# Optimization experiments

Measured on AMD Instinct MI355X. Metric: run time of the kernel, lower is better.

## Reference

```python
import jax, jax.numpy as jnp
import numpy as np

B, S, T = 32, 400, 64
V, E, H = 32000, 256, 512


def _lstm_step(x, h, c, W_ih, W_hh, b):
    # PyTorch LSTM gate order: i, f, g, o
    g = x @ W_ih.T + h @ W_hh.T + b
    i, f, gg, o = jnp.split(g, 4, axis=-1)
    i = jax.nn.sigmoid(i)
    f = jax.nn.sigmoid(f)
    gg = jnp.tanh(gg)
    o = jax.nn.sigmoid(o)
    c_new = f * c + i * gg
    h_new = o * jnp.tanh(c_new)
    return h_new, c_new


def setup_inputs() -> dict:
    key = jax.random.key(0)
    ks = jax.random.split(key, 32)
    d = {}
    d['src'] = jax.random.randint(ks[0], (B, S), 1, V)
    d['src_lengths'] = jnp.full((B,), S, dtype=jnp.int32)
    d['tgt'] = jax.random.randint(ks[1], (B, T), 1, V)
    sc = 0.05
    emb = jax.random.normal(ks[2], (V, E), jnp.float32) * sc
    d['emb'] = emb.at[0].set(0.0)  # padding_idx=0
    d['enc_W_ih_f'] = jax.random.normal(ks[3], (4 * H, E), jnp.float32) * sc
    d['enc_W_hh_f'] = jax.random.normal(ks[4], (4 * H, H), jnp.float32) * sc
    d['enc_b_ih_f'] = jax.random.normal(ks[5], (4 * H,), jnp.float32) * sc
    d['enc_b_hh_f'] = jax.random.normal(ks[6], (4 * H,), jnp.float32) * sc
    d['enc_W_ih_b'] = jax.random.normal(ks[7], (4 * H, E), jnp.float32) * sc
    d['enc_W_hh_b'] = jax.random.normal(ks[8], (4 * H, H), jnp.float32) * sc
    d['enc_b_ih_b'] = jax.random.normal(ks[9], (4 * H,), jnp.float32) * sc
    d['enc_b_hh_b'] = jax.random.normal(ks[10], (4 * H,), jnp.float32) * sc
    d['enc_init_h'] = jax.random.uniform(ks[11], (2, H), jnp.float32, -0.01, 0.01)
    d['enc_init_c'] = jax.random.uniform(ks[12], (2, H), jnp.float32, -0.01, 0.01)
    d['dec_h_W'] = jax.random.normal(ks[13], (H, 2 * H), jnp.float32) * sc
    d['dec_c_W'] = jax.random.normal(ks[14], (H, 2 * H), jnp.float32) * sc
    d['cell_W_ih'] = jax.random.normal(ks[15], (4 * H, E), jnp.float32) * sc
    d['cell_W_hh'] = jax.random.normal(ks[16], (4 * H, H), jnp.float32) * sc
    d['cell_b_ih'] = jax.random.normal(ks[17], (4 * H,), jnp.float32) * sc
    d['cell_b_hh'] = jax.random.normal(ks[18], (4 * H,), jnp.float32) * sc
    d['attn_W'] = jax.random.normal(ks[19], (H, 2 * H), jnp.float32) * sc
    d['attn_b'] = jax.random.normal(ks[20], (H,), jnp.float32) * sc
    d['concat_W'] = jax.random.normal(ks[21], (H, 3 * H), jnp.float32) * sc
    d['concat_b'] = jax.random.normal(ks[22], (H,), jnp.float32) * sc
    d['out_W'] = jax.random.normal(ks[23], (V, H), jnp.float32) * sc
    d['out_b'] = jax.random.normal(ks[24], (V,), jnp.float32) * sc
    return d


def reference(src, src_lengths, tgt, emb,
              enc_W_ih_f, enc_W_hh_f, enc_b_ih_f, enc_b_hh_f,
              enc_W_ih_b, enc_W_hh_b, enc_b_ih_b, enc_b_hh_b,
              enc_init_h, enc_init_c, dec_h_W, dec_c_W,
              cell_W_ih, cell_W_hh, cell_b_ih, cell_b_hh,
              attn_W, attn_b, concat_W, concat_b, out_W, out_b):
    Bs, Ss = src.shape
    Hs = enc_init_h.shape[1]
    xe = emb[src].transpose(1, 0, 2)  # [S, B, E]

    # ---- bi-LSTM encoder (all lengths == S, so packing is identity) ----
    h0f = jnp.broadcast_to(enc_init_h[0], (Bs, Hs))
    c0f = jnp.broadcast_to(enc_init_c[0], (Bs, Hs))
    h0b = jnp.broadcast_to(enc_init_h[1], (Bs, Hs))
    c0b = jnp.broadcast_to(enc_init_c[1], (Bs, Hs))

    def enc_fwd(carry, x):
        h, c = carry
        h, c = _lstm_step(x, h, c, enc_W_ih_f, enc_W_hh_f, enc_b_ih_f + enc_b_hh_f)
        return (h, c), h

    def enc_bwd(carry, x):
        h, c = carry
        h, c = _lstm_step(x, h, c, enc_W_ih_b, enc_W_hh_b, enc_b_ih_b + enc_b_hh_b)
        return (h, c), h

    (hf, cf), out_f = jax.lax.scan(enc_fwd, (h0f, c0f), xe)
    (hb, cb), out_b_seq = jax.lax.scan(enc_bwd, (h0b, c0b), xe[::-1])
    out_b_seq = out_b_seq[::-1]
    enc_outs = jnp.concatenate([out_f, out_b_seq], axis=-1)  # [S, B, 2H]

    # bridge final states to decoder init
    dec_h = jnp.concatenate([hf, hb], axis=-1) @ dec_h_W.T  # [B, H]
    dec_c = jnp.concatenate([cf, cb], axis=-1) @ dec_c_W.T

    mask = jnp.arange(Ss)[None, :] < src_lengths[:, None]  # [B, S]
    attn_keys = enc_outs @ attn_W.T + attn_b  # [S, B, H]

    def dec_step(carry, t_ids):
        h, c = carry
        x = emb[t_ids]  # [B, E]
        h, c = _lstm_step(x, h, c, cell_W_ih, cell_W_hh, cell_b_ih + cell_b_hh)
        scores = jnp.einsum('bh,sbh->bs', h, attn_keys)
        scores = jnp.where(mask, scores, jnp.float32(-1e18))
        w = jax.nn.softmax(scores, axis=1)  # [B, S]
        context = jnp.einsum('bs,sbd->bd', w, enc_outs)  # [B, 2H]
        cc = jnp.tanh(jnp.concatenate([context, h], axis=-1) @ concat_W.T + concat_b)
        logit = jax.nn.log_softmax(cc @ out_W.T + out_b, axis=-1)  # [B, V]
        return (h, c), logit

    _, logits = jax.lax.scan(dec_step, (dec_h, dec_c), tgt.T)  # [T, B, V]
    return logits.transpose(1, 0, 2)  # [B, T, V]
```

## Files before the change

kernel.cpp:

```cpp
#include <hip/hip_runtime.h>
#include <math.h>

#define BB 32
#define SS 400
#define TT 64
#define VV 32000
#define EE 256
#define HH 512

typedef __attribute__((ext_vector_type(4))) float f32x4;
typedef __attribute__((ext_vector_type(8))) short bf16x8t;
typedef __attribute__((ext_vector_type(8))) unsigned short u16x8;
typedef __attribute__((ext_vector_type(4))) unsigned int u32x4;
typedef unsigned long long u64t;

__device__ __forceinline__ ushort f2bf(float x) {
  uint u = __float_as_uint(x);
  return (ushort)((u + 0x7fffu + ((u >> 16) & 1u)) >> 16);
}
__device__ __forceinline__ float bf2f(ushort x) {
  return __uint_as_float(((uint)x) << 16);
}
__device__ __forceinline__ void gload_lds16(const ushort* g, ushort* l) {
  __builtin_amdgcn_global_load_lds(
      (const __attribute__((address_space(1))) void*)g,
      (__attribute__((address_space(3))) void*)l, 16, 0, 0);
}
__device__ __forceinline__ void unpack8(uint4 u, float* f) {
  f[0] = __uint_as_float(u.x << 16); f[1] = __uint_as_float(u.x & 0xffff0000u);
  f[2] = __uint_as_float(u.y << 16); f[3] = __uint_as_float(u.y & 0xffff0000u);
  f[4] = __uint_as_float(u.z << 16); f[5] = __uint_as_float(u.z & 0xffff0000u);
  f[6] = __uint_as_float(u.w << 16); f[7] = __uint_as_float(u.w & 0xffff0000u);
}

__global__ __launch_bounds__(256) void init_all_kernel(
    const float* __restrict__ einh, uint* __restrict__ hge,
    uint* __restrict__ hgb)
{
  int i = blockIdx.x * 256 + threadIdx.x;
  if (i < 4096) {
    int c = (i & 127) * 4;
    uint lo = (uint)f2bf(einh[c]) | ((uint)f2bf(einh[c + 1]) << 16);
    uint hi = (uint)f2bf(einh[c + 2]) | ((uint)f2bf(einh[c + 3]) << 16);
    u32x4 pkt = {lo, hi, 0u, 0u};
    *(u32x4*)(hge + (size_t)i * 4) = pkt;
  } else if (i < 8192) {
    int p = i - 4096;
    int c = HH + (p & 127) * 4;
    uint lo = (uint)f2bf(einh[c]) | ((uint)f2bf(einh[c + 1]) << 16);
    uint hi = (uint)f2bf(einh[c + 2]) | ((uint)f2bf(einh[c + 3]) << 16);
    u32x4 pkt = {lo, hi, 0u, 0u};
    *(u32x4*)(hgb + (size_t)p * 4) = pkt;
  }
}

__global__ __launch_bounds__(256) void f2bf_kernel(
    const float* __restrict__ in, ushort* __restrict__ out, long n)
{
  long step = (long)gridDim.x * 256 * 4;
  for (long i = ((long)blockIdx.x * 256 + threadIdx.x) * 4; i < n; i += step) {
    float4 v = *(const float4*)(in + i);
    ushort4 o;
    o.x = f2bf(v.x); o.y = f2bf(v.y); o.z = f2bf(v.z); o.w = f2bf(v.w);
    *(ushort4*)(out + i) = o;
  }
}

__global__ __launch_bounds__(64) void gather_x_kernel(
    const float* __restrict__ emb, const int* __restrict__ tok, int L,
    ushort* __restrict__ xout)
{
  int row = blockIdx.x;
  int b = row & 31, s = row >> 5;
  int t = tok[b * L + s];
  float4 v = ((const float4*)(emb + (size_t)t * EE))[threadIdx.x];
  ushort4 o;
  o.x = f2bf(v.x); o.y = f2bf(v.y); o.z = f2bf(v.z); o.w = f2bf(v.w);
  ((ushort4*)(xout + (size_t)row * EE))[threadIdx.x] = o;
}

__global__ __launch_bounds__(256) void bias3_kernel(
    const float* a1, const float* a2, const float* b1, const float* b2,
    const float* c1, const float* c2, float* out)
{
  int i = blockIdx.x * 256 + threadIdx.x;
  if (i < 2048) out[i] = a1[i] + a2[i];
  else if (i < 4096) out[i] = b1[i - 2048] + b2[i - 2048];
  else if (i < 6144) out[i] = c1[i - 4096] + c2[i - 4096];
}

__global__ __launch_bounds__(256) void gemm_mfma_kernel(
    const ushort* __restrict__ A, const ushort* __restrict__ B,
    const float* __restrict__ bias, void* __restrict__ Cout,
    int M, int N, int K, int flags)
{
  __shared__ ushort Asub[128 * 32], Bsub[128 * 32];
  int tid = threadIdx.x;
  int w = tid >> 6, l = tid & 63;
  int n0 = blockIdx.x * 128, m0 = blockIdx.y * 128;
  int wm = w >> 1, wn = w & 1;

  int srow = 16 * 2 * w + (l >> 2);
  int scol = (l & 3) * 8;
  const ushort* Ar0 = A + (size_t)(m0 + srow) * K + scol;
  const ushort* Ar1 = Ar0 + (size_t)16 * K;
  const ushort* Br0 = B + (size_t)(n0 + srow) * K + scol;
  const ushort* Br1 = Br0 + (size_t)16 * K;
  ushort* ldsA0 = Asub + (2 * w) * 512;
  ushort* ldsA1 = Asub + (2 * w + 1) * 512;
  ushort* ldsB0 = Bsub + (2 * w) * 512;
  ushort* ldsB1 = Bsub + (2 * w + 1) * 512;

  f32x4 acc[4][4];
  #pragma unroll
  for (int i = 0; i < 4; ++i)
    #pragma unroll
    for (int j = 0; j < 4; ++j)
      acc[i][j] = (f32x4){0.f, 0.f, 0.f, 0.f};

  int lr = l & 15, lkb = (l >> 4) * 8;

  for (int k0 = 0; k0 < K; k0 += 32) {
    gload_lds16(Ar0 + k0, ldsA0);
    gload_lds16(Ar1 + k0, ldsA1);
    gload_lds16(Br0 + k0, ldsB0);
    gload_lds16(Br1 + k0, ldsB1);
    __syncthreads();
    bf16x8t af[4], bfv[4];
    #pragma unroll
    for (int mf = 0; mf < 4; ++mf)
      af[mf] = *(const bf16x8t*)&Asub[(wm * 64 + mf * 16 + lr) * 32 + lkb];
    #pragma unroll
    for (int nf = 0; nf < 4; ++nf)
      bfv[nf] = *(const bf16x8t*)&Bsub[(wn * 64 + nf * 16 + lr) * 32 + lkb];
    #pragma unroll
    for (int mf = 0; mf < 4; ++mf)
      #pragma unroll
      for (int nf = 0; nf < 4; ++nf)
        acc[mf][nf] = __builtin_amdgcn_mfma_f32_16x16x32_bf16(
            af[mf], bfv[nf], acc[mf][nf], 0, 0, 0);
    __syncthreads();
  }

  int lg = l >> 4;
  #pragma unroll
  for (int mf = 0; mf < 4; ++mf) {
    #pragma unroll
    for (int nf = 0; nf < 4; ++nf) {
      int n = n0 + wn * 64 + nf * 16 + lr;
      float bv = bias[n];
      #pragma unroll
      for (int r = 0; r < 4; ++r) {
        int m = m0 + wm * 64 + mf * 16 + lg * 4 + r;
        float v = acc[mf][nf][r] + bv;
        if (flags & 1) v = tanhf(v);
        if (flags & 8) {
          int s = m >> 5, b = m & 31;
          int gate = n >> 9, col = n & 511;
          size_t dst = (((size_t)s * 32 + (col >> 4)) * 32 + b) * 64 +
                       (size_t)(col & 15) * 4 + gate;
          ((ushort*)Cout)[dst] = f2bf(v);
        } else {
          int row = (flags & 2) ? ((m & 31) * TT + (m >> 5)) : m;
          if (flags & 4) ((ushort*)Cout)[(size_t)row * N + n] = f2bf(v);
          else           ((float*)Cout)[(size_t)row * N + n] = v;
        }
      }
    }
  }
}

struct PersistArgs {
  const float* W_hh;
  const ushort* xw;
  uint* hpack;
  const float* c_init_elem;
  const float* c_init_bcast;
  ushort* out_h;
  int out_os, out_ofs;
  int steps, backward;
  float* h_final;
  float* c_final;
};

__global__ __launch_bounds__(256) void lstm_persist_kernel(
    PersistArgs A0, PersistArgs A1, int nblk_dir)
{
  __shared__ ushort ldsW[64 * 512];
  __shared__ ushort ldsH[32 * 512];
  __shared__ ushort ldsX[32 * 64];

  PersistArgs a = ((int)blockIdx.x < nblk_dir) ? A0 : A1;
  int cblk = (int)blockIdx.x % nblk_dir;
  int c0 = cblk * 16;
  int tid = threadIdx.x;
  int w = tid >> 6, l = tid & 63;
  int lr = l & 15, kb = (l >> 4) * 8;
  int g = l & 3;
  int col = c0 + w * 4 + (lr >> 2);
  int n = w * 16 + lr;

  {
    int nn = tid >> 2;
    int kbase = (tid & 3) * 128;
    int rW = (nn & 3) * HH + c0 + (nn >> 2);
    const float4* src = (const float4*)(a.W_hh + (size_t)rW * HH + kbase);
    #pragma unroll
    for (int j = 0; j < 16; ++j) {
      float4 u = src[2 * j], v = src[2 * j + 1];
      u16x8 o;
      o[0] = f2bf(u.x); o[1] = f2bf(u.y); o[2] = f2bf(u.z); o[3] = f2bf(u.w);
      o[4] = f2bf(v.x); o[5] = f2bf(v.y); o[6] = f2bf(v.z); o[7] = f2bf(v.w);
      int k = kbase + j * 8;
      int byte = (nn * 1024 + k * 2) ^ ((nn & 7) << 4);
      *(u16x8*)((char*)ldsW + byte) = o;
    }
  }

  float creg[2][4];
  #pragma unroll
  for (int mf = 0; mf < 2; ++mf)
    #pragma unroll
    for (int r = 0; r < 4; ++r) {
      int b = mf * 16 + (l >> 4) * 4 + r;
      creg[mf][r] = a.c_init_bcast ? a.c_init_bcast[col]
                                   : a.c_init_elem[b * HH + col];
    }
  __syncthreads();

  int prow0 = tid >> 7;
  int pcp4 = tid & 127;

  int s0i = a.backward ? (a.steps - 1) : 0;
  float4 xcur = *(const float4*)(a.xw + ((size_t)s0i * 32 + cblk) * 2048 + tid * 8);
  float4 xnext;

  for (int it = 0; it < a.steps; ++it) {
    int s = a.backward ? (a.steps - 1 - it) : it;
    const uint* hsrc = a.hpack + (size_t)(it & 1) * 4096 * 4;
    uint* hdst = a.hpack + (size_t)((it + 1) & 1) * 4096 * 4;

    u32x4 pv[16];
    {
      int guard = 0;
      while (true) {
        #pragma unroll
        for (int j = 0; j < 16; ++j) {
          const uint* ap = hsrc + (size_t)((prow0 + 2 * j) * 128 + pcp4) * 4;
          asm volatile("global_load_dwordx4 %0, %1, off sc0 sc1"
                       : "=v"(pv[j]) : "v"(ap) : "memory");
        }
        asm volatile("s_waitcnt vmcnt(0)" ::: "memory");
        __builtin_amdgcn_sched_barrier(0);
        uint bad = 0;
        #pragma unroll
        for (int j = 0; j < 16; ++j) bad |= (pv[j][2] ^ (uint)it);
        if (bad == 0) break;
        if (++guard > (1 << 18)) break;
        __builtin_amdgcn_s_sleep(1);
      }
    }
    __syncthreads();

    #pragma unroll
    for (int j = 0; j < 16; ++j) {
      int row = prow0 + 2 * j;
      int byte = (row * 1024 + pcp4 * 8) ^ ((row & 7) << 4);
      *(u64t*)((char*)ldsH + byte) = ((u64t)pv[j][1] << 32) | (u64t)pv[j][0];
    }
    *(float4*)&ldsX[tid * 8] = xcur;
    __syncthreads();

    f32x4 acc0 = (f32x4){0.f, 0.f, 0.f, 0.f};
    f32x4 acc1 = (f32x4){0.f, 0.f, 0.f, 0.f};
    #pragma unroll
    for (int k0 = 0; k0 < HH; k0 += 32) {
      int ka = k0 + kb;
      bf16x8t av0 = *(const bf16x8t*)((const char*)ldsH + ((lr * 1024 + ka * 2) ^ ((lr & 7) << 4)));
      bf16x8t av1 = *(const bf16x8t*)((const char*)ldsH + (((16 + lr) * 1024 + ka * 2) ^ (((16 + lr) & 7) << 4)));
      int wr = w * 16 + lr;
      bf16x8t bv = *(const bf16x8t*)((const char*)ldsW + ((wr * 1024 + ka * 2) ^ ((wr & 7) << 4)));
      acc0 = __builtin_amdgcn_mfma_f32_16x16x32_bf16(av0, bv, acc0, 0, 0, 0);
      acc1 = __builtin_amdgcn_mfma_f32_16x16x32_bf16(av1, bv, acc1, 0, 0, 0);
    }

    u64t pk[2][4];
    #pragma unroll
    for (int mf = 0; mf < 2; ++mf) {
      f32x4 ac = mf ? acc1 : acc0;
      #pragma unroll
      for (int r = 0; r < 4; ++r) {
        int b = mf * 16 + (l >> 4) * 4 + r;
        float v = ac[r] + bf2f(ldsX[b * 64 + n]);
        float b1 = __shfl_xor(v, 1);
        float b2 = __shfl_xor(v, 2);
        float b3 = __shfl_xor(v, 3);
        float hnew = 0.f;
        if (g == 0) {
          float iv = 1.f / (1.f + expf(-v));
          float fv = 1.f / (1.f + expf(-b1));
          float gv = tanhf(b2);
          float ov = 1.f / (1.f + expf(-b3));
          float cnew = fv * creg[mf][r] + iv * gv;
          hnew = ov * tanhf(cnew);
          creg[mf][r] = cnew;
          if (a.h_final && it == a.steps - 1) {
            a.h_final[b * HH + col] = hnew;
            a.c_final[b * HH + col] = cnew;
          }
        }
        uint hu = (uint)f2bf(hnew);
        uint p1 = __shfl_xor(hu, 4);
        uint p2 = __shfl_xor(hu, 8);
        uint p3 = __shfl_xor(p1, 8);
        uint lo = hu | (p1 << 16);
        uint hi = p2 | (p3 << 16);
        pk[mf][r] = ((u64t)hi << 32) | (u64t)lo;
      }
    }

    if ((l & 15) == 0 && it + 1 < a.steps) {
      int cp4w = cblk * 4 + w;
      #pragma unroll
      for (int mf = 0; mf < 2; ++mf)
        #pragma unroll
        for (int r = 0; r < 4; ++r) {
          int b = mf * 16 + (l >> 4) * 4 + r;
          u32x4 pkt;
          pkt[0] = (uint)pk[mf][r];
          pkt[1] = (uint)(pk[mf][r] >> 32);
          pkt[2] = (uint)(it + 1);
          pkt[3] = 0u;
          uint* dp = hdst + (size_t)(b * 128 + cp4w) * 4;
          asm volatile("global_store_dwordx4 %0, %1, off sc0 sc1"
                       :: "v"(dp), "v"(pkt) : "memory");
        }
    }

    if ((l & 15) == 0) {
      #pragma unroll
      for (int mf = 0; mf < 2; ++mf)
        #pragma unroll
        for (int r = 0; r < 4; ++r) {
          int b = mf * 16 + (l >> 4) * 4 + r;
          *(u64t*)(a.out_h + (size_t)s * BB * a.out_os + b * a.out_os +
                   a.out_ofs + c0 + w * 4) = pk[mf][r];
        }
    }
    if (it + 1 < a.steps) {
      int sn = a.backward ? (a.steps - 2 - it) : (it + 1);
      const ushort* xp = a.xw + ((size_t)sn * 32 + cblk) * 2048 + tid * 8;
      asm volatile("global_load_dwordx4 %0, %1, off"
                   : "=v"(xnext) : "v"(xp) : "memory");
    }
    xcur = xnext;
  }
}

__global__ __launch_bounds__(256) void dec_init_kernel(
    const float* __restrict__ hf, const float* __restrict__ hb,
    const float* __restrict__ cf, const float* __restrict__ cb,
    const float* __restrict__ Wh, const float* __restrict__ Wc,
    uint* __restrict__ dh_pack, float* __restrict__ dc)
{
  int b = blockIdx.x;
  __shared__ float hcat[2 * HH], ccat[2 * HH];
  __shared__ ushort dhs[HH];
  int tid = threadIdx.x;
  for (int i = tid; i < HH; i += 256) {
    hcat[i] = hf[b * HH + i]; hcat[HH + i] = hb[b * HH + i];
    ccat[i] = cf[b * HH + i]; ccat[HH + i] = cb[b * HH + i];
  }
  __syncthreads();
  for (int col = tid; col < HH; col += 256) {
    const float4* wh = (const float4*)(Wh + (size_t)col * (2 * HH));
    const float4* wc = (const float4*)(Wc + (size_t)col * (2 * HH));
    float ah = 0.f, acv = 0.f;
    #pragma unroll 4
    for (int k4 = 0; k4 < (2 * HH) / 4; ++k4) {
      float4 h4 = *(const float4*)&hcat[k4 * 4];
      float4 w4 = wh[k4];
      ah += h4.x * w4.x + h4.y * w4.y + h4.z * w4.z + h4.w * w4.w;
      float4 c4 = *(const float4*)&ccat[k4 * 4];
      float4 v4 = wc[k4];
      acv += c4.x * v4.x + c4.y * v4.y + c4.z * v4.z + c4.w * v4.w;
    }
    dhs[col] = f2bf(ah);
    dc[b * HH + col] = acv;
  }
  __syncthreads();
  if (tid < 128) {
    int c = tid * 4;
    uint lo = (uint)dhs[c] | ((uint)dhs[c + 1] << 16);
    uint hi = (uint)dhs[c + 2] | ((uint)dhs[c + 3] << 16);
    u32x4 pkt = {lo, hi, 0u, 0u};
    *(u32x4*)(dh_pack + (size_t)(b * 128 + tid) * 4) = pkt;
  }
}

__global__ __launch_bounds__(256) void scores_kernel(
    const ushort* __restrict__ keys_bf, const ushort* __restrict__ dhall,
    const int* __restrict__ slen, float* __restrict__ sc)
{
  int b = blockIdx.x & 31, s0 = ((int)blockIdx.x >> 5) * 16;
  __shared__ ushort ldsD[64][520];
  __shared__ ushort ldsK[16][520];
  int tid = threadIdx.x;
  #pragma unroll
  for (int j = 0; j < 16; ++j) {
    int ci = tid + 256 * j;
    int row = ci >> 6, c8 = (ci & 63) * 8;
    *(u16x8*)&ldsD[row][c8] = *(const u16x8*)(dhall + ((size_t)row * BB + b) * HH + c8);
  }
  #pragma unroll
  for (int j = 0; j < 4; ++j) {
    int ci = tid + 256 * j;
    int row = ci >> 6, c8 = (ci & 63) * 8;
    *(u16x8*)&ldsK[row][c8] = *(const u16x8*)(keys_bf + ((size_t)(s0 + row) * BB + b) * HH + c8);
  }
  __syncthreads();

  int sl = tid & 15, tq = tid >> 4;
  float acc[4] = {0.f, 0.f, 0.f, 0.f};
  for (int k8 = 0; k8 < 64; ++k8) {
    float kv[8];
    unpack8(*(const uint4*)&ldsK[sl][k8 * 8], kv);
    #pragma unroll
    for (int j = 0; j < 4; ++j) {
      float dv[8];
      unpack8(*(const uint4*)&ldsD[tq * 4 + j][k8 * 8], dv);
      #pragma unroll
      for (int e = 0; e < 8; ++e) acc[j] += kv[e] * dv[e];
    }
  }
  int s = s0 + sl;
  int len = slen[b];
  #pragma unroll
  for (int j = 0; j < 4; ++j) {
    int t = tq * 4 + j;
    sc[((size_t)t * BB + b) * SS + s] = (s < len) ? acc[j] : -1e18f;
  }
}

__global__ __launch_bounds__(64) void softmax_kernel(
    const float* __restrict__ sc, ushort* __restrict__ wbf)
{
  int row = blockIdx.x;
  int tid = threadIdx.x;
  float v[7];
  float m = -3e38f;
  #pragma unroll
  for (int j = 0; j < 7; ++j) {
    int s = tid + 64 * j;
    v[j] = (s < SS) ? sc[(size_t)row * SS + s] : -3e38f;
    m = fmaxf(m, v[j]);
  }
  #pragma unroll
  for (int o = 32; o; o >>= 1) m = fmaxf(m, __shfl_xor(m, o));
  float ssum = 0.f;
  float p[7];
  #pragma unroll
  for (int j = 0; j < 7; ++j) {
    int s = tid + 64 * j;
    p[j] = (s < SS) ? expf(v[j] - m) : 0.f;
    ssum += p[j];
  }
  #pragma unroll
  for (int o = 32; o; o >>= 1) ssum += __shfl_xor(ssum, o);
  float inv = 1.f / ssum;
  #pragma unroll
  for (int j = 0; j < 7; ++j) {
    int s = tid + 64 * j;
    if (s < 416) wbf[(size_t)row * 416 + s] = (s < SS) ? f2bf(p[j] * inv) : (ushort)0;
  }
}

__global__ __launch_bounds__(256) void context_kernel(
    const ushort* __restrict__ wbf, const ushort* __restrict__ enc,
    const ushort* __restrict__ dhall, ushort* __restrict__ catb)
{
  int b = blockIdx.x, ch = blockIdx.y;
  int tid = threadIdx.x;
  if (ch >= 16) {
    int c0 = (ch - 16) * 64;
    #pragma unroll
    for (int j = 0; j < 2; ++j) {
      int ci = tid + 256 * j;
      int t = ci >> 3, u = ci & 7;
      *(u16x8*)(catb + ((size_t)t * BB + b) * 1536 + 1024 + c0 + u * 8) =
          *(const u16x8*)(dhall + ((size_t)t * BB + b) * HH + c0 + u * 8);
    }
    return;
  }
  int d0 = ch * 64;
  __shared__ ushort ldsWt[64][424];
  for (int ci = tid; ci < 64 * 52; ci += 256) {
    int t = ci / 52, u = ci % 52;
    *(u16x8*)&ldsWt[t][u * 8] = *(const u16x8*)(wbf + (size_t)(t * BB + b) * 416 + u * 8);
  }
  __syncthreads();

  int d = d0 + (tid & 63), tq = tid >> 6;
  float acc16[16];
  #pragma unroll
  for (int i = 0; i < 16; ++i) acc16[i] = 0.f;

  for (int s8 = 0; s8 < 50; ++s8) {
    float ev[8];
    #pragma unroll
    for (int e = 0; e < 8; ++e)
      ev[e] = bf2f(enc[((size_t)(s8 * 8 + e) * BB + b) * 1024 + d]);
    #pragma unroll
    for (int i = 0; i < 16; ++i) {
      float wv[8];
      unpack8(*(const uint4*)&ldsWt[tq * 16 + i][s8 * 8], wv);
      #pragma unroll
      for (int e = 0; e < 8; ++e) acc16[i] += wv[e] * ev[e];
    }
  }
  #pragma unroll
  for (int i = 0; i < 16; ++i) {
    int t = tq * 16 + i;
    catb[((size_t)t * BB + b) * 1536 + d] = f2bf(acc16[i]);
  }
}

__global__ __launch_bounds__(1024) void logsoftmax_kernel(float* __restrict__ out)
{
  int r = blockIdx.x;
  __shared__ float row[VV];
  __shared__ float red[16];
  int tid = threadIdx.x;
  float4* p = (float4*)(out + (size_t)r * VV);
  float4* rp = (float4*)row;
  float m = -3e38f;
  #pragma unroll
  for (int j = 0; j < 8; ++j) {
    int i = tid + 1024 * j;
    if (i < VV / 4) {
      float4 v = p[i];
      rp[i] = v;
      m = fmaxf(m, fmaxf(fmaxf(v.x, v.y), fmaxf(v.z, v.w)));
    }
  }
  #pragma unroll
  for (int o = 32; o; o >>= 1) m = fmaxf(m, __shfl_xor(m, o));
  if ((tid & 63) == 0) red[tid >> 6] = m;
  __syncthreads();
  float mm = red[0];
  #pragma unroll
  for (int i = 1; i < 16; ++i) mm = fmaxf(mm, red[i]);
  __syncthreads();
  float ssum = 0.f;
  #pragma unroll
  for (int j = 0; j < 8; ++j) {
    int i = tid + 1024 * j;
    if (i < VV / 4) {
      float4 v = rp[i];
      ssum += expf(v.x - mm) + expf(v.y - mm) + expf(v.z - mm) + expf(v.w - mm);
    }
  }
  #pragma unroll
  for (int o = 32; o; o >>= 1) ssum += __shfl_xor(ssum, o);
  if ((tid & 63) == 0) red[tid >> 6] = ssum;
  __syncthreads();
  float st = red[0];
  #pragma unroll
  for (int i = 1; i < 16; ++i) st += red[i];
  st = mm + logf(st);
  #pragma unroll
  for (int j = 0; j < 8; ++j) {
    int i = tid + 1024 * j;
    if (i < VV / 4) {
      float4 v = rp[i];
      v.x -= st; v.y -= st; v.z -= st; v.w -= st;
      p[i] = v;
    }
  }
}

extern "C" void kernel_launch(void* const* d_in, const int* in_sizes, int n_in,
                              void* d_out, int out_size, void* d_ws, size_t ws_size,
                              hipStream_t stream)
{
  (void)in_sizes; (void)n_in; (void)out_size; (void)ws_size;
  const int*   src  = (const int*)d_in[0];
  const int*   slen = (const int*)d_in[1];
  const int*   tgt  = (const int*)d_in[2];
  const float* emb  = (const float*)d_in[3];
  const float* eWif = (const float*)d_in[4];
  const float* eWhf = (const float*)d_in[5];
  const float* ebif = (const float*)d_in[6];
  const float* ebhf = (const float*)d_in[7];
  const float* eWib = (const float*)d_in[8];
  const float* eWhb = (const float*)d_in[9];
  const float* ebib = (const float*)d_in[10];
  const float* ebhb = (const float*)d_in[11];
  const float* einh = (const float*)d_in[12];
  const float* einc = (const float*)d_in[13];
  const float* dhW  = (const float*)d_in[14];
  const float* dcW  = (const float*)d_in[15];
  const float* cWi  = (const float*)d_in[16];
  const float* cWh  = (const float*)d_in[17];
  const float* cbi  = (const float*)d_in[18];
  const float* cbh  = (const float*)d_in[19];
  const float* aW   = (const float*)d_in[20];
  const float* abv  = (const float*)d_in[21];
  const float* ccW  = (const float*)d_in[22];
  const float* ccbv = (const float*)d_in[23];
  const float* oW   = (const float*)d_in[24];
  const float* obv  = (const float*)d_in[25];
  float* out = (float*)d_out;
  float* ws  = (float*)d_ws;

  size_t off = 0;
  ushort* enc_bf  = (ushort*)(ws + off); off += (size_t)SS * BB * 1024 / 2;
  ushort* keys_bf = (ushort*)(ws + off); off += (size_t)SS * BB * HH / 2;
  ushort* dhall_bf= (ushort*)(ws + off); off += (size_t)TT * BB * HH / 2;
  ushort* catb_bf = (ushort*)(ws + off); off += (size_t)TT * BB * 1536 / 2;
  ushort* ccv_bf  = (ushort*)(ws + off); off += (size_t)TT * BB * HH / 2;
  float*  scbuf   = ws + off;            off += (size_t)TT * BB * SS;
  ushort* w_bf    = (ushort*)(ws + off); off += (size_t)TT * BB * 416 / 2;
  ushort* xe_bf   = (ushort*)(ws + off); off += (size_t)SS * BB * EE / 2;
  ushort* xd_bf   = (ushort*)(ws + off); off += (size_t)TT * BB * EE / 2;
  ushort* xWf_bf  = (ushort*)(ws + off); off += (size_t)SS * BB * 2048 / 2;
  ushort* xWb_bf  = (ushort*)(ws + off); off += (size_t)SS * BB * 2048 / 2;
  ushort* xWd_bf  = (ushort*)(ws + off); off += (size_t)TT * BB * 2048 / 2;
  ushort* oW_bf   = (ushort*)(ws + off); off += (size_t)VV * HH / 2;
  ushort* aW_bf   = (ushort*)(ws + off); off += (size_t)HH * 1024 / 2;
  ushort* ccW_bf  = (ushort*)(ws + off); off += (size_t)HH * 1536 / 2;
  ushort* eWif_bf = (ushort*)(ws + off); off += (size_t)2048 * EE / 2;
  ushort* eWib_bf = (ushort*)(ws + off); off += (size_t)2048 * EE / 2;
  ushort* cWi_bf  = (ushort*)(ws + off); off += (size_t)2048 * EE / 2;
  uint* hge_pack = (uint*)(ws + off); off += (size_t)2 * 4096 * 4;
  uint* hgb_pack = (uint*)(ws + off); off += (size_t)2 * 4096 * 4;
  uint* hdec_pack= (uint*)(ws + off); off += (size_t)2 * 4096 * 4;
  float* bias3 = ws + off; off += 3 * 2048;
  float* hf_f  = ws + off; off += BB * HH;
  float* hb_f  = ws + off; off += BB * HH;
  float* cf_f  = ws + off; off += BB * HH;
  float* cb_f  = ws + off; off += BB * HH;
  float* dcb   = ws + off; off += BB * HH;

  hipMemsetAsync(hge_pack, 0, (size_t)3 * 2 * 4096 * 16, stream);

  init_all_kernel<<<64, 256, 0, stream>>>(einh, hge_pack, hgb_pack);

  f2bf_kernel<<<2048, 256, 0, stream>>>(oW, oW_bf, (long)VV * HH);
  f2bf_kernel<<<512, 256, 0, stream>>>(aW, aW_bf, (long)HH * 1024);
  f2bf_kernel<<<512, 256, 0, stream>>>(ccW, ccW_bf, (long)HH * 1536);
  f2bf_kernel<<<512, 256, 0, stream>>>(eWif, eWif_bf, (long)2048 * EE);
  f2bf_kernel<<<512, 256, 0, stream>>>(eWib, eWib_bf, (long)2048 * EE);
  f2bf_kernel<<<512, 256, 0, stream>>>(cWi, cWi_bf, (long)2048 * EE);
  bias3_kernel<<<24, 256, 0, stream>>>(ebif, ebhf, ebib, ebhb, cbi, cbh, bias3);

  gather_x_kernel<<<SS * BB, 64, 0, stream>>>(emb, src, SS, xe_bf);
  gather_x_kernel<<<TT * BB, 64, 0, stream>>>(emb, tgt, TT, xd_bf);
  gemm_mfma_kernel<<<dim3(2048 / 128, (SS * BB) / 128), 256, 0, stream>>>(
      xe_bf, eWif_bf, bias3, xWf_bf, SS * BB, 2048, EE, 8);
  gemm_mfma_kernel<<<dim3(2048 / 128, (SS * BB) / 128), 256, 0, stream>>>(
      xe_bf, eWib_bf, bias3 + 2048, xWb_bf, SS * BB, 2048, EE, 8);
  gemm_mfma_kernel<<<dim3(2048 / 128, (TT * BB) / 128), 256, 0, stream>>>(
      xd_bf, cWi_bf, bias3 + 4096, xWd_bf, TT * BB, 2048, EE, 8);

  {
    PersistArgs af, ab;
    af.W_hh = eWhf; af.xw = xWf_bf; af.hpack = hge_pack;
    af.c_init_elem = nullptr; af.c_init_bcast = einc;
    af.out_h = enc_bf; af.out_os = 1024; af.out_ofs = 0;
    af.steps = SS; af.backward = 0;
    af.h_final = hf_f; af.c_final = cf_f;
    ab = af;
    ab.W_hh = eWhb; ab.xw = xWb_bf; ab.hpack = hgb_pack;
    ab.c_init_bcast = einc + HH;
    ab.out_ofs = HH; ab.backward = 1;
    ab.h_final = hb_f; ab.c_final = cb_f;
    lstm_persist_kernel<<<64, 256, 0, stream>>>(af, ab, 32);
  }

  dec_init_kernel<<<BB, 256, 0, stream>>>(hf_f, hb_f, cf_f, cb_f, dhW, dcW,
                                          hdec_pack, dcb);
  {
    PersistArgs ad;
    ad.W_hh = cWh; ad.xw = xWd_bf; ad.hpack = hdec_pack;
    ad.c_init_elem = dcb; ad.c_init_bcast = nullptr;
    ad.out_h = dhall_bf; ad.out_os = HH; ad.out_ofs = 0;
    ad.steps = TT; ad.backward = 0;
    ad.h_final = nullptr; ad.c_final = nullptr;
    lstm_persist_kernel<<<32, 256, 0, stream>>>(ad, ad, 32);
  }

  gemm_mfma_kernel<<<dim3(HH / 128, (SS * BB) / 128), 256, 0, stream>>>(
      enc_bf, aW_bf, abv, keys_bf, SS * BB, HH, 1024, 4);

  scores_kernel<<<32 * 25, 256, 0, stream>>>(keys_bf, dhall_bf, slen, scbuf);
  softmax_kernel<<<TT * BB, 64, 0, stream>>>(scbuf, w_bf);
  context_kernel<<<dim3(BB, 24), 256, 0, stream>>>(w_bf, enc_bf, dhall_bf, catb_bf);

  gemm_mfma_kernel<<<dim3(HH / 128, (TT * BB) / 128), 256, 0, stream>>>(
      catb_bf, ccW_bf, ccbv, ccv_bf, TT * BB, HH, 1536, 1 | 4);
  gemm_mfma_kernel<<<dim3(VV / 128, (TT * BB) / 128), 256, 0, stream>>>(
      ccv_bf, oW_bf, obv, out, TT * BB, VV, HH, 2);

  logsoftmax_kernel<<<TT * BB, 1024, 0, stream>>>(out);
}
```

Baseline: 3.548 ms.

## Use fast exp math, spread gate activations across lanes, poll per-row in encoder

Replaces expf/tanhf with __expf-based sigmoid and tanh in the LSTM cell and the softmax/log-softmax kernels. Each lane now applies its own gate activation before the shuffles, so the transcendental work is spread across four lanes instead of done serially on one. The spin-wait on the h exchange now issues all loads once and re-polls only the rows whose flag is stale, instead of reloading all sixteen. Fast exp lowers accuracy slightly, and the poll change alters synchronisation latency on the serial recurrence.

```diff
diff --git a/kernel.cpp b/kernel.cpp
--- a/kernel.cpp
+++ b/kernel.cpp
@@ -20,6 +20,12 @@
 }
 __device__ __forceinline__ float bf2f(ushort x) {
   return __uint_as_float(((uint)x) << 16);
+}
+__device__ __forceinline__ float fsigmoid(float x) {
+  return 1.f / (1.f + __expf(-x));
+}
+__device__ __forceinline__ float ftanh(float x) {
+  return 1.f - 2.f / (__expf(2.f * x) + 1.f);
 }
 __device__ __forceinline__ void gload_lds16(const ushort* g, ushort* l) {
   __builtin_amdgcn_global_load_lds(
@@ -241,23 +247,25 @@
     uint* hdst = a.hpack + (size_t)((it + 1) & 1) * 4096 * 4;
 
     u32x4 pv[16];
-    {
+    #pragma unroll
+    for (int j = 0; j < 16; ++j) {
+      const uint* ap = hsrc + (size_t)((prow0 + 2 * j) * 128 + pcp4) * 4;
+      asm volatile("global_load_dwordx4 %0, %1, off sc0 sc1"
+                   : "=v"(pv[j]) : "v"(ap) : "memory");
+    }
+    asm volatile("s_waitcnt vmcnt(0)" ::: "memory");
+    __builtin_amdgcn_sched_barrier(0);
+    #pragma unroll
+    for (int j = 0; j < 16; ++j) {
+      const uint* ap = hsrc + (size_t)((prow0 + 2 * j) * 128 + pcp4) * 4;
       int guard = 0;
-      while (true) {
-        #pragma unroll
-        for (int j = 0; j < 16; ++j) {
-          const uint* ap = hsrc + (size_t)((prow0 + 2 * j) * 128 + pcp4) * 4;
-          asm volatile("global_load_dwordx4 %0, %1, off sc0 sc1"
-                       : "=v"(pv[j]) : "v"(ap) : "memory");
-        }
-        asm volatile("s_waitcnt vmcnt(0)" ::: "memory");
+      while (pv[j][2] != (uint)it) {
+        __builtin_amdgcn_s_sleep(1);
+        asm volatile("global_load_dwordx4 %0, %1, off sc0 sc1\n\t"
+                     "s_waitcnt vmcnt(0)"
+                     : "=v"(pv[j]) : "v"(ap) : "memory");
         __builtin_amdgcn_sched_barrier(0);
-        uint bad = 0;
-        #pragma unroll
-        for (int j = 0; j < 16; ++j) bad |= (pv[j][2] ^ (uint)it);
-        if (bad == 0) break;
-        if (++guard > (1 << 18)) break;
-        __builtin_amdgcn_s_sleep(1);
+        if (++guard > (1 << 20)) break;
       }
     }
     __syncthreads();
@@ -292,17 +300,15 @@
       for (int r = 0; r < 4; ++r) {
         int b = mf * 16 + (l >> 4) * 4 + r;
         float v = ac[r] + bf2f(ldsX[b * 64 + n]);
-        float b1 = __shfl_xor(v, 1);
-        float b2 = __shfl_xor(v, 2);
-        float b3 = __shfl_xor(v, 3);
+        float av = (g == 2) ? ftanh(v) : fsigmoid(v);
+        float a1 = __shfl_xor(av, 1);
+        float a2 = __shfl_xor(av, 2);
+        float a3 = __shfl_xor(av, 3);
         float hnew = 0.f;
         if (g == 0) {
-          float iv = 1.f / (1.f + expf(-v));
-          float fv = 1.f / (1.f + expf(-b1));
-          float gv = tanhf(b2);
-          float ov = 1.f / (1.f + expf(-b3));
+          float iv = av, fv = a1, gv = a2, ov = a3;
           float cnew = fv * creg[mf][r] + iv * gv;
-          hnew = ov * tanhf(cnew);
+          hnew = ov * ftanh(cnew);
           creg[mf][r] = cnew;
           if (a.h_final && it == a.steps - 1) {
             a.h_final[b * HH + col] = hnew;
@@ -462,7 +468,7 @@
   #pragma unroll
   for (int j = 0; j < 7; ++j) {
     int s = tid + 64 * j;
-    p[j] = (s < SS) ? expf(v[j] - m) : 0.f;
+    p[j] = (s < SS) ? __expf(v[j] - m) : 0.f;
     ssum += p[j];
   }
   #pragma unroll
@@ -557,7 +563,7 @@
     int i = tid + 1024 * j;
     if (i < VV / 4) {
       float4 v = rp[i];
-      ssum += expf(v.x - mm) + expf(v.y - mm) + expf(v.z - mm) + expf(v.w - mm);
+      ssum += __expf(v.x - mm) + __expf(v.y - mm) + __expf(v.z - mm) + __expf(v.w - mm);
     }
   }
   #pragma unroll
```

New measurement: 4.688 ms. +32.1%, slower.
